# Kernel optimization log

Measured on AMD Instinct MI355X. Metric: run time of the kernel, lower is better.

## Reference

```python
import jax, jax.numpy as jnp
import numpy as np
from jax import lax

FPLANE = 64
T = 8          # num_segments
HEADS = 4
EPS = 1e-5


def _conv2d(x, w, b):
    # x: [N,C,H,W], w: [O,I,kh,kw]
    y = lax.conv_general_dilated(x, w, (1, 1), 'SAME',
                                 dimension_numbers=('NCHW', 'OIHW', 'NCHW'))
    return y + b[None, :, None, None]


def _conv3d_grouped(x, w, b, groups):
    # x: [N,C,D,H,W], w: [O, C//groups, kd,kh,kw]
    y = lax.conv_general_dilated(x, w, (1, 1, 1), 'SAME',
                                 dimension_numbers=('NCDHW', 'OIDHW', 'NCDHW'),
                                 feature_group_count=groups)
    return y + b[None, :, None, None, None]


def setup_inputs() -> dict:
    key = jax.random.key(0)
    ks = jax.random.split(key, 5)
    N, C, H, W = T * 16, FPLANE, 56, 56
    x = jax.random.normal(ks[0], (N, C, H, W), dtype=jnp.float32)
    attn_w = jax.random.normal(ks[1], (HEADS, C, 3, 3), dtype=jnp.float32) * 0.05
    attn_b = jax.random.normal(ks[2], (HEADS,), dtype=jnp.float32) * 0.05
    bn_gamma = jnp.ones((C,), dtype=jnp.float32)
    bn_beta = jnp.zeros((C,), dtype=jnp.float32)
    conv3d_w = jax.random.normal(ks[3], (2, C // 2, 3, 3, 3), dtype=jnp.float32) * 0.05
    conv3d_b = jax.random.normal(ks[4], (2,), dtype=jnp.float32) * 0.05
    return {'x': x, 'attn_w': attn_w, 'attn_b': attn_b,
            'bn_gamma': bn_gamma, 'bn_beta': bn_beta,
            'conv3d_w': conv3d_w, 'conv3d_b': conv3d_b}


def reference(x, attn_w, attn_b, bn_gamma, bn_beta, conv3d_w, conv3d_b):
    N, C, H, W = x.shape
    B = N // T
    half = C // 2
    quarter = C // 4

    # spatial attention: conv2d -> ReLU -> Sigmoid, per-head gating
    attn = jax.nn.sigmoid(jax.nn.relu(_conv2d(x, attn_w, attn_b)))  # [N,HEADS,H,W]
    xh = x.reshape(N, HEADS, C // HEADS, H, W) * attn[:, :, None]
    x2 = xh.reshape(N, C, H, W)

    # [B*T,C,H,W] -> [B,C,T,H,W]
    x5 = x2.reshape(B, T, C, H, W).transpose(0, 2, 1, 3, 4)

    # BatchNorm3d (training-mode batch statistics) + ReLU
    mean = jnp.mean(x5, axis=(0, 2, 3, 4), keepdims=True)
    var = jnp.var(x5, axis=(0, 2, 3, 4), keepdims=True)
    x_bn = (x5 - mean) * lax.rsqrt(var + EPS)
    x_bn = x_bn * bn_gamma[None, :, None, None, None] + bn_beta[None, :, None, None, None]
    x_bn_relu = jax.nn.relu(x_bn)

    # grouped conv3d gate (2 groups, 1 output channel each), tanh
    gate = jnp.tanh(_conv3d_grouped(x_bn_relu, conv3d_w, conv3d_b, groups=2))  # [B,2,T,H,W]
    g1 = gate[:, 0:1]
    g2 = gate[:, 1:2]

    x_g1 = x5[:, :half]
    x_g2 = x5[:, half:]
    y1 = g1 * x_g1
    y2 = g2 * x_g2
    r1 = x_g1 - y1
    r2 = x_g2 - y2

    pad_t = ((0, 0), (0, 0), (0, 1), (0, 0), (0, 0))
    pad_b = ((0, 0), (0, 0), (1, 0), (0, 0), (0, 0))
    y1 = jnp.pad(y1[:, :, 1:], pad_t) + r1   # left shift in time, zero pad
    y2 = jnp.pad(y2[:, :, :-1], pad_b) + r2  # right shift in time, zero pad

    # interleave sub-halves: view [B,2,C/4,T,H,W] -> permute -> [B,C/2,T,H,W]
    def interleave(y):
        return (y.reshape(B, 2, quarter, T, H, W)
                 .transpose(0, 2, 1, 3, 4, 5)
                 .reshape(B, half, T, H, W))

    y = jnp.concatenate([interleave(y1), interleave(y2)], axis=1)  # [B,C,T,H,W]
    return y.transpose(0, 2, 1, 3, 4).reshape(N, C, H, W)
```

## Files before the change

kernel.cpp:

```cpp
#include <hip/hip_runtime.h>
#include <hip/hip_bf16.h>

#define HW 3136
#define CTOT 64
#define NTOT 128
#define BB 16
#define TTT 8

static __device__ __forceinline__ float bf2f(unsigned short u) {
    union { unsigned int ui; float f; } v;
    v.ui = ((unsigned int)u) << 16;
    return v.f;
}
static __device__ __forceinline__ unsigned short f2bf(float f) {
    union { float f; unsigned int u; } v;
    v.f = f;
    unsigned int u = v.u;
    unsigned int r = (u + 0x7fffu + ((u >> 16) & 1u)) >> 16;
    return (unsigned short)r;
}

__global__ void k_repack(const float* __restrict__ aw, float* __restrict__ wpk,
                         float* __restrict__ stats) {
    const int idx = blockIdx.x * 256 + threadIdx.x;
    if (idx < 2048) stats[idx] = 0.f;
    if (idx >= 2304) return;
    const int hd = idx & 3;
    const int kw = (idx >> 2) % 3;
    const int dh = (idx / 12) % 3;
    const int c = idx / 36;
    wpk[idx] = aw[hd * 576 + c * 9 + dh * 3 + kw];
}

__global__ __launch_bounds__(128) void k_attn(const float* __restrict__ x,
                                              const float* __restrict__ wpk,
                                              const float* __restrict__ ab,
                                              float* __restrict__ attn,
                                              float* __restrict__ stats) {
    const int tile = blockIdx.x % 49;
    const int n = blockIdx.x / 49;
    const int chunk = threadIdx.x >> 4;
    const int qi = threadIdx.x & 15;
    const int quad = tile * 16 + qi;
    const int q = quad % 14;
    const int h = quad / 14;
    const int w0 = q * 4;

    __shared__ float smem[2304];
    __shared__ float4 abuf[4][16];
    float (*l)[16][17] = (float (*)[16][17])smem;

    const float* xn = x + (size_t)n * CTOT * HW;
    const int c0 = chunk * 8;

    auto loadrows = [&](int c, float r[3][6]) {
#pragma unroll
        for (int dh = 0; dh < 3; ++dh) {
            const int hh = h + dh - 1;
            const bool v = (hh >= 0) && (hh < 56);
            const float* row = xn + c * HW + (v ? hh : h) * 56 + w0;
            const float m = v ? 1.f : 0.f;
            const float4 mid = *(const float4*)row;
            const float e0 = row[(q > 0) ? -1 : 0] * ((q > 0) ? m : 0.f);
            const float e5 = row[(q < 13) ? 4 : 3] * ((q < 13) ? m : 0.f);
            r[dh][0] = e0;
            r[dh][1] = mid.x * m; r[dh][2] = mid.y * m;
            r[dh][3] = mid.z * m; r[dh][4] = mid.w * m;
            r[dh][5] = e5;
        }
    };

    float bufA[3][6], bufB[3][6];
    loadrows(c0, bufA);

#pragma unroll
    for (int i = 0; i < 18; ++i) smem[threadIdx.x + i * 128] = wpk[threadIdx.x + i * 128];
    __syncthreads();

    float acc[4][4];
#pragma unroll
    for (int hd = 0; hd < 4; ++hd)
#pragma unroll
        for (int j = 0; j < 4; ++j) acc[hd][j] = 0.f;

#pragma unroll
    for (int i = 0; i < 8; ++i) {
        float (*cur)[6] = (i & 1) ? bufB : bufA;
        float (*nxt)[6] = (i & 1) ? bufA : bufB;
        if (i < 7) loadrows(c0 + i + 1, nxt);

        const int c = c0 + i;
#pragma unroll
        for (int dh = 0; dh < 3; ++dh) {
            const float* wb = &smem[c * 36 + dh * 12];
            const float4 wk0 = *(const float4*)(wb);
            const float4 wk1 = *(const float4*)(wb + 4);
            const float4 wk2 = *(const float4*)(wb + 8);
#pragma unroll
            for (int j = 0; j < 4; ++j) {
                const float a0 = cur[dh][j], a1 = cur[dh][j + 1], a2 = cur[dh][j + 2];
                acc[0][j] = fmaf(a0, wk0.x, fmaf(a1, wk1.x, fmaf(a2, wk2.x, acc[0][j])));
                acc[1][j] = fmaf(a0, wk0.y, fmaf(a1, wk1.y, fmaf(a2, wk2.y, acc[1][j])));
                acc[2][j] = fmaf(a0, wk0.z, fmaf(a1, wk1.z, fmaf(a2, wk2.z, acc[2][j])));
                acc[3][j] = fmaf(a0, wk0.w, fmaf(a1, wk1.w, fmaf(a2, wk2.w, acc[3][j])));
            }
        }
    }

    __syncthreads();

    float* mine = &l[chunk][qi][0];
#pragma unroll
    for (int hd = 0; hd < 4; ++hd)
#pragma unroll
        for (int j = 0; j < 4; ++j) mine[hd * 4 + j] = acc[hd][j];
    __syncthreads();

    if (threadIdx.x < 64) {
        const int hd = threadIdx.x >> 4;
        const int rq = threadIdx.x & 15;
        float s0 = ab[hd], s1 = s0, s2 = s0, s3 = s0;
#pragma unroll
        for (int cch = 0; cch < 8; ++cch) {
            const float* p = &l[cch][rq][hd * 4];
            s0 += p[0]; s1 += p[1]; s2 += p[2]; s3 += p[3];
        }
        float4 o;
        o.x = s0 > 0.f ? 1.f / (1.f + __expf(-s0)) : 0.5f;
        o.y = s1 > 0.f ? 1.f / (1.f + __expf(-s1)) : 0.5f;
        o.z = s2 > 0.f ? 1.f / (1.f + __expf(-s2)) : 0.5f;
        o.w = s3 > 0.f ? 1.f / (1.f + __expf(-s3)) : 0.5f;
        *(float4*)(attn + (size_t)(n * 4 + hd) * HW + (tile * 16 + rq) * 4) = o;
        abuf[hd][rq] = o;
    }
    __syncthreads();

    const int head = chunk >> 1;
    const float4 a4 = abuf[head][qi];
    float s[8], sq[8];
#pragma unroll
    for (int i = 0; i < 8; ++i) {
        const float4 xv = *(const float4*)(xn + (size_t)(c0 + i) * HW + quad * 4);
        const float v0 = xv.x * a4.x;
        const float v1 = xv.y * a4.y;
        const float v2 = xv.z * a4.z;
        const float v3 = xv.w * a4.w;
        s[i] = v0 + v1 + v2 + v3;
        sq[i] = v0 * v0 + v1 * v1 + v2 * v2 + v3 * v3;
    }
#pragma unroll
    for (int i = 0; i < 8; ++i) { mine[i] = s[i]; mine[8 + i] = sq[i]; }
    __syncthreads();
    {
        const int ch2 = threadIdx.x >> 4;
        const int k = threadIdx.x & 15;
        float t = 0.f;
#pragma unroll
        for (int qq = 0; qq < 16; ++qq) t += l[ch2][qq][k];
        const int cc = ch2 * 8 + (k & 7);
        const int rep = blockIdx.x & 15;
        atomicAdd(&stats[rep * 128 + (k >> 3) * 64 + cc], t);
    }
}

__global__ __launch_bounds__(256) void k_xbnr(const float* __restrict__ x,
                                              const float* __restrict__ attn,
                                              const float* __restrict__ stats,
                                              const float* __restrict__ gamma,
                                              const float* __restrict__ beta,
                                              unsigned short* __restrict__ xbnr) {
    const int s = blockIdx.x & 7;
    const int n = blockIdx.x >> 3;
    const int base_sp = s * 392;

    __shared__ float al[4 * 392];
    __shared__ float ssl[128];
    for (int i = threadIdx.x; i < 392; i += 256) {
        const int hd = i / 98;
        const int j = i - hd * 98;
        ((float4*)al)[hd * 98 + j] =
            *(const float4*)(attn + (size_t)(n * 4 + hd) * HW + base_sp + j * 4);
    }
    if (threadIdx.x < 64) {
        const int c = threadIdx.x;
        float S = 0.f, Q = 0.f;
#pragma unroll
        for (int r = 0; r < 16; ++r) {
            S += stats[r * 128 + c];
            Q += stats[r * 128 + 64 + c];
        }
        const float cnt = 401408.0f;
        const float mean = S / cnt;
        const float var = Q / cnt - mean * mean;
        const float scale = gamma[c] * rsqrtf(var + 1e-5f);
        ssl[c] = scale;
        ssl[64 + c] = beta[c] - mean * scale;
    }
    __syncthreads();

    for (int wi = threadIdx.x; wi < 6272; wi += 256) {
        const int c = wi / 98;
        const int j = wi - c * 98;
        const float sc = ssl[c], sh = ssl[64 + c];
        const float4 xv = *(const float4*)(x + (size_t)(n * 64 + c) * HW + base_sp + j * 4);
        const float4 av = ((const float4*)al)[(c >> 4) * 98 + j];
        ushort4 o;
        o.x = f2bf(fmaxf(fmaf(xv.x * av.x, sc, sh), 0.f));
        o.y = f2bf(fmaxf(fmaf(xv.y * av.y, sc, sh), 0.f));
        o.z = f2bf(fmaxf(fmaf(xv.z * av.z, sc, sh), 0.f));
        o.w = f2bf(fmaxf(fmaf(xv.w * av.w, sc, sh), 0.f));
        *(ushort4*)(xbnr + (size_t)(n * 64 + c) * HW + base_sp + j * 4) = o;
    }
}

__global__ __launch_bounds__(128) void k_conv3d(const unsigned short* __restrict__ xbnr,
                                                const float* __restrict__ w3,
                                                const float* __restrict__ b3,
                                                float* __restrict__ gate) {
    const int tile = blockIdx.x % 49;
    const int oc = (blockIdx.x / 49) & 1;
    const int b = blockIdx.x / 98;
    const int chunk = threadIdx.x >> 4;
    const int qi = threadIdx.x & 15;
    const int quad = tile * 16 + qi;
    const int q = quad % 14;
    const int h = quad / 14;
    const int w0 = q * 4;

    __shared__ float wlds[864];
    for (int i = threadIdx.x; i < 864; i += 128) wlds[i] = w3[oc * 864 + i];
    __syncthreads();

    float acc[8][4];
#pragma unroll
    for (int t = 0; t < 8; ++t)
#pragma unroll
        for (int j = 0; j < 4; ++j) acc[t][j] = 0.f;

    const int ic0 = chunk * 4;
    for (int ic = ic0; ic < ic0 + 4; ++ic) {
        const int c = oc * 32 + ic;
        const unsigned short* cbase = xbnr + (size_t)(b * 8 * 64 + c) * HW;
        const float* wic = &wlds[ic * 27];
#pragma unroll
        for (int tt = 0; tt < 8; ++tt) {
            const unsigned short* plane = cbase + (size_t)tt * (64 * HW);
#pragma unroll
            for (int dh = 0; dh < 3; ++dh) {
                const int hh = h + dh - 1;
                if (hh < 0 || hh >= 56) continue;
                const unsigned short* row = plane + hh * 56 + w0;
                const ushort4 mid = *(const ushort4*)row;
                const float f0 = (q > 0) ? bf2f(row[-1]) : 0.f;
                const float f1 = bf2f(mid.x), f2 = bf2f(mid.y);
                const float f3 = bf2f(mid.z), f4 = bf2f(mid.w);
                const float f5 = (q < 13) ? bf2f(row[4]) : 0.f;
#pragma unroll
                for (int dt = 0; dt < 3; ++dt) {
                    const int t = tt + 1 - dt;
                    if (t < 0 || t > 7) continue;
                    const float* wp = wic + dt * 9 + dh * 3;
                    const float wa = wp[0], wb = wp[1], wc = wp[2];
                    acc[t][0] = fmaf(f0, wa, fmaf(f1, wb, fmaf(f2, wc, acc[t][0])));
                    acc[t][1] = fmaf(f1, wa, fmaf(f2, wb, fmaf(f3, wc, acc[t][1])));
                    acc[t][2] = fmaf(f2, wa, fmaf(f3, wb, fmaf(f4, wc, acc[t][2])));
                    acc[t][3] = fmaf(f3, wa, fmaf(f4, wb, fmaf(f5, wc, acc[t][3])));
                }
            }
        }
    }

    __shared__ float4 l4[8 * 16 * 9];
    float4* mine = &l4[(chunk * 16 + qi) * 9];
#pragma unroll
    for (int t = 0; t < 8; ++t) {
        float4 v;
        v.x = acc[t][0]; v.y = acc[t][1]; v.z = acc[t][2]; v.w = acc[t][3];
        mine[t] = v;
    }
    __syncthreads();

    const int rt = threadIdx.x >> 4;
    const int rq = threadIdx.x & 15;
    float4 s = l4[(0 * 16 + rq) * 9 + rt];
#pragma unroll
    for (int c = 1; c < 8; ++c) {
        const float4 v = l4[(c * 16 + rq) * 9 + rt];
        s.x += v.x; s.y += v.y; s.z += v.z; s.w += v.w;
    }
    const float bb = b3[oc];
    float4 o;
    o.x = tanhf(s.x + bb);
    o.y = tanhf(s.y + bb);
    o.z = tanhf(s.z + bb);
    o.w = tanhf(s.w + bb);
    const int outquad = tile * 16 + rq;
    *(float4*)(gate + (size_t)((b * 2 + oc) * 8 + rt) * HW + outquad * 4) = o;
}

__global__ __launch_bounds__(448) void k_final(const float* __restrict__ x,
                                               const float* __restrict__ attn,
                                               const float* __restrict__ gate,
                                               float* __restrict__ out) {
    const int hg = blockIdx.x & 1;
    const int h = (blockIdx.x >> 1) % 56;
    const int b = blockIdx.x / 112;
    const int q = threadIdx.x % 14;
    const int col = threadIdx.x / 14;
    const int co = hg * 32 + col;
    const int sp = h * 56 + q * 4;

    int cs;
    if (co < 32) {
        cs = ((co & 1) << 4) | (co >> 1);
    } else {
        const int cc = co - 32;
        cs = 32 + (((cc & 1) << 4) | (cc >> 1));
    }
    const int grp = hg;
    const int head = cs >> 4;

    float4 x2v[8], g[8];
#pragma unroll
    for (int t = 0; t < 8; ++t) {
        const int n = b * 8 + t;
        const float4 xv = *(const float4*)(x + (size_t)(n * 64 + cs) * HW + sp);
        const float4 av = *(const float4*)(attn + (size_t)(n * 4 + head) * HW + sp);
        const float4 gv = *(const float4*)(gate + (size_t)((b * 2 + grp) * 8 + t) * HW + sp);
        x2v[t].x = xv.x * av.x;
        x2v[t].y = xv.y * av.y;
        x2v[t].z = xv.z * av.z;
        x2v[t].w = xv.w * av.w;
        g[t] = gv;
    }
#pragma unroll
    for (int t = 0; t < 8; ++t) {
        float4 o;
        o.x = x2v[t].x * (1.f - g[t].x);
        o.y = x2v[t].y * (1.f - g[t].y);
        o.z = x2v[t].z * (1.f - g[t].z);
        o.w = x2v[t].w * (1.f - g[t].w);
        if (grp == 0) {
            if (t < 7) {
                o.x += x2v[t + 1].x * g[t + 1].x;
                o.y += x2v[t + 1].y * g[t + 1].y;
                o.z += x2v[t + 1].z * g[t + 1].z;
                o.w += x2v[t + 1].w * g[t + 1].w;
            }
        } else {
            if (t > 0) {
                o.x += x2v[t - 1].x * g[t - 1].x;
                o.y += x2v[t - 1].y * g[t - 1].y;
                o.z += x2v[t - 1].z * g[t - 1].z;
                o.w += x2v[t - 1].w * g[t - 1].w;
            }
        }
        *(float4*)(out + (size_t)((b * 8 + t) * 64 + co) * HW + sp) = o;
    }
}

extern "C" void kernel_launch(void* const* d_in, const int* in_sizes, int n_in,
                              void* d_out, int out_size, void* d_ws, size_t ws_size,
                              hipStream_t stream) {
    const float* x = (const float*)d_in[0];
    const float* aw = (const float*)d_in[1];
    const float* ab = (const float*)d_in[2];
    const float* gamma = (const float*)d_in[3];
    const float* beta = (const float*)d_in[4];
    const float* w3 = (const float*)d_in[5];
    const float* b3 = (const float*)d_in[6];
    float* out = (float*)d_out;

    char* ws = (char*)d_ws;
    unsigned short* xbnr = (unsigned short*)ws;
    float* attn = (float*)(ws + 51380224);
    float* gate = (float*)(ws + 57802752);
    float* stats = (float*)(ws + 57802752);
    float* wpk = (float*)(ws + 61015040);

    k_repack<<<9, 256, 0, stream>>>(aw, wpk, stats);
    k_attn<<<6272, 128, 0, stream>>>(x, wpk, ab, attn, stats);
    k_xbnr<<<1024, 256, 0, stream>>>(x, attn, stats, gamma, beta, xbnr);
    k_conv3d<<<1568, 128, 0, stream>>>(xbnr, w3, b3, gate);
    k_final<<<1792, 448, 0, stream>>>(x, attn, gate, out);
}
```

Before: 360.8 us.

## Fuse conv3d gate computation with final shift-and-interleave output kernel

The conv3d kernel no longer writes the gate tensor to global memory. Each block keeps its gate tile in shared memory, reusing the weight buffer, and then produces the final shifted, interleaved output for its spatial tile and group. The gate now travels along time in a register carry instead of being reloaded. This removes one kernel launch and a gate write plus read, but the conv3d kernel now also streams x and attn for 32 channels. That may lengthen each block and hurt occupancy or latency hiding.

```diff
diff --git a/kernel.cpp b/kernel.cpp
--- a/kernel.cpp
+++ b/kernel.cpp
@@ -213,10 +213,12 @@
     }
 }
 
-__global__ __launch_bounds__(128) void k_conv3d(const unsigned short* __restrict__ xbnr,
-                                                const float* __restrict__ w3,
-                                                const float* __restrict__ b3,
-                                                float* __restrict__ gate) {
+__global__ __launch_bounds__(128) void k_gate(const unsigned short* __restrict__ xbnr,
+                                              const float* __restrict__ w3,
+                                              const float* __restrict__ b3,
+                                              const float* __restrict__ x,
+                                              const float* __restrict__ attn,
+                                              float* __restrict__ out) {
     const int tile = blockIdx.x % 49;
     const int oc = (blockIdx.x / 49) & 1;
     const int b = blockIdx.x / 98;
@@ -228,6 +230,7 @@
     const int w0 = q * 4;
 
     __shared__ float wlds[864];
+    float4* gl = (float4*)wlds;
     for (int i = threadIdx.x; i < 864; i += 128) wlds[i] = w3[oc * 864 + i];
     __syncthreads();
 
@@ -280,82 +283,66 @@
     }
     __syncthreads();
 
-    const int rt = threadIdx.x >> 4;
-    const int rq = threadIdx.x & 15;
-    float4 s = l4[(0 * 16 + rq) * 9 + rt];
-#pragma unroll
-    for (int c = 1; c < 8; ++c) {
-        const float4 v = l4[(c * 16 + rq) * 9 + rt];
-        s.x += v.x; s.y += v.y; s.z += v.z; s.w += v.w;
-    }
-    const float bb = b3[oc];
-    float4 o;
-    o.x = tanhf(s.x + bb);
-    o.y = tanhf(s.y + bb);
-    o.z = tanhf(s.z + bb);
-    o.w = tanhf(s.w + bb);
-    const int outquad = tile * 16 + rq;
-    *(float4*)(gate + (size_t)((b * 2 + oc) * 8 + rt) * HW + outquad * 4) = o;
-}
-
-__global__ __launch_bounds__(448) void k_final(const float* __restrict__ x,
-                                               const float* __restrict__ attn,
-                                               const float* __restrict__ gate,
-                                               float* __restrict__ out) {
-    const int hg = blockIdx.x & 1;
-    const int h = (blockIdx.x >> 1) % 56;
-    const int b = blockIdx.x / 112;
-    const int q = threadIdx.x % 14;
-    const int col = threadIdx.x / 14;
-    const int co = hg * 32 + col;
-    const int sp = h * 56 + q * 4;
-
-    int cs;
-    if (co < 32) {
-        cs = ((co & 1) << 4) | (co >> 1);
-    } else {
-        const int cc = co - 32;
-        cs = 32 + (((cc & 1) << 4) | (cc >> 1));
-    }
-    const int grp = hg;
-    const int head = cs >> 4;
-
-    float4 x2v[8], g[8];
-#pragma unroll
-    for (int t = 0; t < 8; ++t) {
-        const int n = b * 8 + t;
-        const float4 xv = *(const float4*)(x + (size_t)(n * 64 + cs) * HW + sp);
-        const float4 av = *(const float4*)(attn + (size_t)(n * 4 + head) * HW + sp);
-        const float4 gv = *(const float4*)(gate + (size_t)((b * 2 + grp) * 8 + t) * HW + sp);
-        x2v[t].x = xv.x * av.x;
-        x2v[t].y = xv.y * av.y;
-        x2v[t].z = xv.z * av.z;
-        x2v[t].w = xv.w * av.w;
-        g[t] = gv;
-    }
-#pragma unroll
-    for (int t = 0; t < 8; ++t) {
+    {
+        const int rt = threadIdx.x >> 4;
+        const int rq = threadIdx.x & 15;
+        float4 s = l4[(0 * 16 + rq) * 9 + rt];
+#pragma unroll
+        for (int c = 1; c < 8; ++c) {
+            const float4 v = l4[(c * 16 + rq) * 9 + rt];
+            s.x += v.x; s.y += v.y; s.z += v.z; s.w += v.w;
+        }
+        const float bb = b3[oc];
         float4 o;
-        o.x = x2v[t].x * (1.f - g[t].x);
-        o.y = x2v[t].y * (1.f - g[t].y);
-        o.z = x2v[t].z * (1.f - g[t].z);
-        o.w = x2v[t].w * (1.f - g[t].w);
+        o.x = tanhf(s.x + bb);
+        o.y = tanhf(s.y + bb);
+        o.z = tanhf(s.z + bb);
+        o.w = tanhf(s.w + bb);
+        gl[rt * 16 + rq] = o;
+    }
+    __syncthreads();
+
+    const int grp = oc;
+#pragma unroll
+    for (int k = 0; k < 4; ++k) {
+        const int cell = threadIdx.x + k * 128;
+        const int co = cell >> 4;
+        const int qq = cell & 15;
+        const int sp = (tile * 16 + qq) * 4;
+        const int cs = grp * 32 + (((co & 1) << 4) | (co >> 1));
+        const int head = cs >> 4;
+        const int co_out = grp * 32 + co;
+
+        float4 yc; yc.x = 0.f; yc.y = 0.f; yc.z = 0.f; yc.w = 0.f;
         if (grp == 0) {
-            if (t < 7) {
-                o.x += x2v[t + 1].x * g[t + 1].x;
-                o.y += x2v[t + 1].y * g[t + 1].y;
-                o.z += x2v[t + 1].z * g[t + 1].z;
-                o.w += x2v[t + 1].w * g[t + 1].w;
+            for (int t = 7; t >= 0; --t) {
+                const int n = b * 8 + t;
+                const float4 xv = *(const float4*)(x + (size_t)(n * 64 + cs) * HW + sp);
+                const float4 av = *(const float4*)(attn + (size_t)(n * 4 + head) * HW + sp);
+                const float4 g = gl[t * 16 + qq];
+                float4 x2, y, o2;
+                x2.x = xv.x * av.x; x2.y = xv.y * av.y; x2.z = xv.z * av.z; x2.w = xv.w * av.w;
+                y.x = x2.x * g.x;   y.y = x2.y * g.y;   y.z = x2.z * g.z;   y.w = x2.w * g.w;
+                o2.x = x2.x - y.x + yc.x; o2.y = x2.y - y.y + yc.y;
+                o2.z = x2.z - y.z + yc.z; o2.w = x2.w - y.w + yc.w;
+                yc = y;
+                *(float4*)(out + (size_t)(n * 64 + co_out) * HW + sp) = o2;
             }
         } else {
-            if (t > 0) {
-                o.x += x2v[t - 1].x * g[t - 1].x;
-                o.y += x2v[t - 1].y * g[t - 1].y;
-                o.z += x2v[t - 1].z * g[t - 1].z;
-                o.w += x2v[t - 1].w * g[t - 1].w;
+            for (int t = 0; t < 8; ++t) {
+                const int n = b * 8 + t;
+                const float4 xv = *(const float4*)(x + (size_t)(n * 64 + cs) * HW + sp);
+                const float4 av = *(const float4*)(attn + (size_t)(n * 4 + head) * HW + sp);
+                const float4 g = gl[t * 16 + qq];
+                float4 x2, y, o2;
+                x2.x = xv.x * av.x; x2.y = xv.y * av.y; x2.z = xv.z * av.z; x2.w = xv.w * av.w;
+                y.x = x2.x * g.x;   y.y = x2.y * g.y;   y.z = x2.z * g.z;   y.w = x2.w * g.w;
+                o2.x = x2.x - y.x + yc.x; o2.y = x2.y - y.y + yc.y;
+                o2.z = x2.z - y.z + yc.z; o2.w = x2.w - y.w + yc.w;
+                yc = y;
+                *(float4*)(out + (size_t)(n * 64 + co_out) * HW + sp) = o2;
             }
         }
-        *(float4*)(out + (size_t)((b * 8 + t) * 64 + co) * HW + sp) = o;
     }
 }
 
@@ -374,13 +361,11 @@
     char* ws = (char*)d_ws;
     unsigned short* xbnr = (unsigned short*)ws;
     float* attn = (float*)(ws + 51380224);
-    float* gate = (float*)(ws + 57802752);
     float* stats = (float*)(ws + 57802752);
     float* wpk = (float*)(ws + 61015040);
 
     k_repack<<<9, 256, 0, stream>>>(aw, wpk, stats);
     k_attn<<<6272, 128, 0, stream>>>(x, wpk, ab, attn, stats);
     k_xbnr<<<1024, 256, 0, stream>>>(x, attn, stats, gamma, beta, xbnr);
-    k_conv3d<<<1568, 128, 0, stream>>>(xbnr, w3, b3, gate);
-    k_final<<<1792, 448, 0, stream>>>(x, attn, gate, out);
-}
+    k_gate<<<1568, 128, 0, stream>>>(xbnr, w3, b3, x, attn, out);
+}
```

New measurement: 344.8 us. -4.4%, faster.
